# Kernel tuning notes

Measured on AMD Instinct MI355X. Metric: run time of the kernel, lower is better.

## Reference

```python
import jax, jax.numpy as jnp
import numpy as np

B, N, K = 32, 128, 16
F_ATOM, F_NEI, D = 256, 256, 256
H = 4
DK = D // H
NEG = -1e9
EPS = 1e-5
SLOPE = 0.2  # LeakyReLU slope (GAT convention)


def setup_inputs() -> dict:
    key = jax.random.key(0)
    ks = jax.random.split(key, 10)
    atom_feature = jax.random.normal(ks[0], (B, N, F_ATOM), jnp.float32)
    atom_neighbor_feature = jax.random.normal(ks[1], (B, N, K, F_NEI), jnp.float32)
    keep = (jax.random.uniform(ks[2], (B, N, K, 1)) < 0.8).astype(jnp.float32)
    atom_softmax_mask = (keep - 1.0) * (-NEG)  # 0 where valid, -1e9 where padded
    atom_attend_mask = keep
    s_a = 1.0 / np.sqrt(F_ATOM)
    s_n = 1.0 / np.sqrt(F_NEI)
    s_al = 1.0 / np.sqrt(DK)
    return {
        "atom_feature": atom_feature,
        "atom_neighbor_feature": atom_neighbor_feature,
        "atom_softmax_mask": atom_softmax_mask,
        "atom_attend_mask": atom_attend_mask,
        "W_a": jax.random.uniform(ks[3], (D, F_ATOM), jnp.float32, -s_a, s_a),
        "b_a": jnp.zeros((D,), jnp.float32),
        "W_n": jax.random.uniform(ks[4], (D, F_NEI), jnp.float32, -s_n, s_n),
        "b_n": jnp.zeros((D,), jnp.float32),
        "w_align": jax.random.uniform(ks[5], (DK,), jnp.float32, -s_al, s_al),
        "b_align": jnp.zeros((), jnp.float32),
        "ln_gamma": jnp.ones((D,), jnp.float32),
        "ln_beta": jnp.zeros((D,), jnp.float32),
    }


def reference(atom_feature, atom_neighbor_feature, atom_softmax_mask,
              atom_attend_mask, W_a, b_a, W_n, b_n, w_align, b_align,
              ln_gamma, ln_beta):
    # Linear projections (dropout is identity at inference)
    af = jnp.einsum('bnf,df->bnd', atom_feature, W_a) + b_a            # [B,N,D]
    nf = jnp.einsum('bnkf,df->bnkd', atom_neighbor_feature, W_n) + b_n  # [B,N,K,D]
    b, n, k, d = nf.shape
    afh = af.reshape(b, n, 1, H, DK)      # broadcast over neighbor axis
    nfh = nf.reshape(b, n, k, H, DK)
    # GATV2: act(Wa x_i + Wn x_j) . a
    feat = jax.nn.leaky_relu(afh + nfh, SLOPE)                          # [B,N,K,H,DK]
    score = jnp.einsum('bnkhd,d->bnkh', feat, w_align) + b_align        # [B,N,K,H]
    score = score + atom_softmax_mask                                   # [B,N,K,1] -> bcast over H
    attw = jax.nn.softmax(score, axis=2)                                # softmax over neighbors
    attw = attw * atom_attend_mask                                      # zero out padded neighbors
    ctx = jnp.einsum('bnkh,bnkhd->bnhd', attw, nfh).reshape(b, n, d)    # weighted sum
    # LayerNorm
    mu = jnp.mean(ctx, axis=-1, keepdims=True)
    var = jnp.mean(jnp.square(ctx - mu), axis=-1, keepdims=True)
    out = (ctx - mu) * jax.lax.rsqrt(var + EPS) * ln_gamma + ln_beta
    return out
```

## Files before the change

### kernel.cpp

```cpp
#include <hip/hip_runtime.h>
#include <hip/hip_bf16.h>


typedef float f32x4 __attribute__((ext_vector_type(4)));
typedef __bf16 bf16x8 __attribute__((ext_vector_type(8)));

__device__ __forceinline__ unsigned short f2bf(float x) {
    unsigned int u = __float_as_uint(x);
    u += 0x7FFFu + ((u >> 16) & 1u);
    return (unsigned short)(u >> 16);
}

__device__ __forceinline__ void gemm_tile(const float4* __restrict__ src4,
                                          const unsigned short* __restrict__ w,
                                          char* lds_a, f32x4 acc[2][4]) {
    const int tid = threadIdx.x;
#pragma unroll
    for (int j = 0; j < 8; ++j) {
        const int idx4 = tid + j * 256;
        const float4 v = src4[idx4];
        const int r = idx4 >> 6;
        const int byt = (idx4 & 63) * 8;
        ushort4 h;
        h.x = f2bf(v.x); h.y = f2bf(v.y); h.z = f2bf(v.z); h.w = f2bf(v.w);
        *(ushort4*)(lds_a + r * 512 + (byt ^ ((r & 7) << 4))) = h;
    }
    __syncthreads();
    const int lane = tid & 63;
    const int wv   = tid >> 6;
    const int l15  = lane & 15;
    const int lg   = lane >> 4;
#pragma unroll
    for (int kk = 0; kk < 8; ++kk) {
        const int f = kk * 32 + lg * 8;
        bf16x8 afrag[2];
#pragma unroll
        for (int mi = 0; mi < 2; ++mi) {
            const int r = mi * 16 + l15;
            afrag[mi] = *(const bf16x8*)(lds_a + r * 512 + ((f * 2) ^ ((r & 7) << 4)));
        }
#pragma unroll
        for (int ni = 0; ni < 4; ++ni) {
            const int d = wv * 64 + ni * 16 + l15;
            const bf16x8 bfrag = *(const bf16x8*)(w + d * 256 + f);
#pragma unroll
            for (int mi = 0; mi < 2; ++mi)
                acc[mi][ni] = __builtin_amdgcn_mfma_f32_16x16x32_bf16(
                    afrag[mi], bfrag, acc[mi][ni], 0, 0, 0);
        }
    }
}

__global__ __launch_bounds__(256) void conv_w(const float4* __restrict__ wa,
                                              const float4* __restrict__ wn,
                                              ushort4* __restrict__ owa,
                                              ushort4* __restrict__ own) {
    const int i = blockIdx.x * 256 + threadIdx.x;
    const float4 a = wa[i], n = wn[i];
    ushort4 ha, hn;
    ha.x = f2bf(a.x); ha.y = f2bf(a.y); ha.z = f2bf(a.z); ha.w = f2bf(a.w);
    hn.x = f2bf(n.x); hn.y = f2bf(n.y); hn.z = f2bf(n.z); hn.w = f2bf(n.w);
    owa[i] = ha; own[i] = hn;
}

__global__ __launch_bounds__(256) void proj_atoms(const float* __restrict__ atomf,
                                                  const unsigned short* __restrict__ wa,
                                                  const float* __restrict__ b_a,
                                                  float* __restrict__ af) {
    __shared__ char lds[32 * 512];
    f32x4 acc[2][4];
#pragma unroll
    for (int mi = 0; mi < 2; ++mi)
#pragma unroll
        for (int ni = 0; ni < 4; ++ni)
#pragma unroll
            for (int j = 0; j < 4; ++j) acc[mi][ni][j] = 0.f;
    gemm_tile((const float4*)(atomf + blockIdx.x * 32 * 256), wa, lds, acc);
    const int lane = threadIdx.x & 63, wv = threadIdx.x >> 6;
    const int l15 = lane & 15, lg = lane >> 4;
#pragma unroll
    for (int ni = 0; ni < 4; ++ni) {
        const int d = wv * 64 + ni * 16 + l15;
        const float b = b_a[d];
#pragma unroll
        for (int mi = 0; mi < 2; ++mi)
#pragma unroll
            for (int j = 0; j < 4; ++j)
                af[(blockIdx.x * 32 + mi * 16 + lg * 4 + j) * 256 + d] = acc[mi][ni][j] + b;
    }
}

struct Smem2 {
    union {
        char  a[32 * 512];
        float nf[32][260];
    } u;
    float af[2][256];
    float wal[64];
    float attw[2][4][16];
    float red[4][2][2];
};

__global__ __launch_bounds__(256) void gat_fused(
        const float* __restrict__ nei, const float* __restrict__ afbuf,
        const unsigned short* __restrict__ wn, const float* __restrict__ b_n,
        const float* __restrict__ smask, const float* __restrict__ amask,
        const float* __restrict__ w_align, const float* __restrict__ b_align,
        const float* __restrict__ gamma, const float* __restrict__ beta,
        float* __restrict__ out) {
    __shared__ Smem2 s;
    const int tid = threadIdx.x;
    const int p = blockIdx.x;

    s.af[0][tid] = afbuf[p * 512 + tid];
    s.af[1][tid] = afbuf[p * 512 + 256 + tid];
    if (tid < 64) s.wal[tid] = w_align[tid];

    f32x4 acc[2][4];
#pragma unroll
    for (int mi = 0; mi < 2; ++mi)
#pragma unroll
        for (int ni = 0; ni < 4; ++ni)
#pragma unroll
            for (int j = 0; j < 4; ++j) acc[mi][ni][j] = 0.f;

    gemm_tile((const float4*)(nei + (size_t)p * 32 * 256), wn, s.u.a, acc);
    __syncthreads();

    const int lane = tid & 63, wv = tid >> 6, l15 = lane & 15, lg = lane >> 4;
#pragma unroll
    for (int ni = 0; ni < 4; ++ni) {
        const int d = wv * 64 + ni * 16 + l15;
        const float bn = b_n[d];
#pragma unroll
        for (int mi = 0; mi < 2; ++mi)
#pragma unroll
            for (int j = 0; j < 4; ++j)
                s.u.nf[mi * 16 + lg * 4 + j][d] = acc[mi][ni][j] + bn;
    }
    __syncthreads();

    if (tid < 128) {
        const int a = tid >> 6, h = (tid >> 4) & 3, k = tid & 15;
        const float* afr = &s.af[a][h * 64];
        const float* nfr = &s.u.nf[a * 16 + k][h * 64];
        float sc = 0.f;
#pragma unroll
        for (int dk = 0; dk < 64; ++dk) {
            float x = afr[dk] + nfr[dk];
            x = (x >= 0.f) ? x : 0.2f * x;
            sc = fmaf(x, s.wal[dk], sc);
        }
        sc += b_align[0] + smask[p * 32 + a * 16 + k];
        float mx = sc;
#pragma unroll
        for (int o = 1; o < 16; o <<= 1) mx = fmaxf(mx, __shfl_xor(mx, o));
        const float e = __expf(sc - mx);
        float sm = e;
#pragma unroll
        for (int o = 1; o < 16; o <<= 1) sm += __shfl_xor(sm, o);
        s.attw[a][h][k] = (e / sm) * amask[p * 32 + a * 16 + k];
    }
    __syncthreads();

    const int d = tid;
    const float g = gamma[d], be = beta[d];
    const int h = d >> 6;
#pragma unroll
    for (int a = 0; a < 2; ++a) {
        float c = 0.f;
#pragma unroll
        for (int k = 0; k < 16; ++k)
            c = fmaf(s.attw[a][h][k], s.u.nf[a * 16 + k][d], c);
        float sm = c, sq = c * c;
#pragma unroll
        for (int o = 1; o < 64; o <<= 1) {
            sm += __shfl_xor(sm, o);
            sq += __shfl_xor(sq, o);
        }
        if (lane == 0) { s.red[wv][a][0] = sm; s.red[wv][a][1] = sq; }
        __syncthreads();
        float ts = 0.f, tq = 0.f;
#pragma unroll
        for (int q = 0; q < 4; ++q) { ts += s.red[q][a][0]; tq += s.red[q][a][1]; }
        const float mu = ts * (1.f / 256.f);
        float var = tq * (1.f / 256.f) - mu * mu;
        var = fmaxf(var, 0.f);
        out[(p * 2 + a) * 256 + d] = (c - mu) * rsqrtf(var + 1e-5f) * g + be;
        __syncthreads();
    }
}

extern "C" void kernel_launch(void* const* d_in, const int* in_sizes, int n_in,
                              void* d_out, int out_size, void* d_ws, size_t ws_size,
                              hipStream_t stream) {
    const float* atomf = (const float*)d_in[0];
    const float* nei   = (const float*)d_in[1];
    const float* smask = (const float*)d_in[2];
    const float* amask = (const float*)d_in[3];
    const float* Wa    = (const float*)d_in[4];
    const float* ba    = (const float*)d_in[5];
    const float* Wn    = (const float*)d_in[6];
    const float* bn    = (const float*)d_in[7];
    const float* wal   = (const float*)d_in[8];
    const float* bal   = (const float*)d_in[9];
    const float* gam   = (const float*)d_in[10];
    const float* bet   = (const float*)d_in[11];
    float* out = (float*)d_out;

    char* ws = (char*)d_ws;
    float*          af_buf = (float*)ws;
    unsigned short* wa_bf  = (unsigned short*)(ws + 4194304);
    unsigned short* wn_bf  = (unsigned short*)(ws + 4194304 + 131072);

    hipLaunchKernelGGL(conv_w, dim3(64), dim3(256), 0, stream,
                       (const float4*)Wa, (const float4*)Wn,
                       (ushort4*)wa_bf, (ushort4*)wn_bf);
    hipLaunchKernelGGL(proj_atoms, dim3(128), dim3(256), 0, stream,
                       atomf, wa_bf, ba, af_buf);
    hipLaunchKernelGGL(gat_fused, dim3(2048), dim3(256), 0, stream,
                       nei, af_buf, wn_bf, bn, smask, amask, wal, bal, gam, bet, out);
}
```

Before: 162.3 us.

## Fuse atom projection into GAT kernel with pre-swizzled bf16 weight fragments

Drops the separate proj_atoms kernel and its global af buffer. Each block now projects its two atom rows in an extra MFMA row-tile, reading bf16 weights stored in MFMA fragment order and prefetching the next k-step's fragments into registers. It also vectorises the score loop with float4 LDS reads, merges the two LayerNorm passes so fewer barriers are needed, and pads the nf rows. The costs are extra MFMA work on a mostly empty 16-row tile (only 2 rows are valid) and higher register pressure, with a launch-bounds occupancy hint of 3.

```diff
diff --git a/kernel.cpp b/kernel.cpp
--- a/kernel.cpp
+++ b/kernel.cpp
@@ -11,10 +11,50 @@
     return (unsigned short)(u >> 16);
 }
 
-__device__ __forceinline__ void gemm_tile(const float4* __restrict__ src4,
-                                          const unsigned short* __restrict__ w,
-                                          char* lds_a, f32x4 acc[2][4]) {
+__global__ __launch_bounds__(256) void conv_w(const float* __restrict__ wa,
+                                              const float* __restrict__ wn,
+                                              unsigned short* __restrict__ owa,
+                                              unsigned short* __restrict__ own) {
+    const int g = blockIdx.x * 256 + threadIdx.x;
+    const float* src = (g & 8192) ? wn : wa;
+    unsigned short* dst = (g & 8192) ? own : owa;
+    const int c = g & 8191;
+    const int lane = c & 63, ni = (c >> 6) & 3, kk = (c >> 8) & 7, wv = c >> 11;
+    const int d = wv * 64 + ni * 16 + (lane & 15);
+    const int f = kk * 32 + (lane >> 4) * 8;
+    const float* sp = src + d * 256 + f;
+    unsigned short h[8];
+#pragma unroll
+    for (int j = 0; j < 8; ++j) h[j] = f2bf(sp[j]);
+    *(uint4*)(dst + c * 8) = *(const uint4*)h;
+}
+
+struct Smem2 {
+    union {
+        char  a[48 * 512];
+        float nf[32][264];
+    } u;
+    float af[2][256];
+    float wal[64];
+    float attw[2][4][16];
+    float red[4][2][2];
+};
+
+__global__ __launch_bounds__(256, 3) void gat_fused(
+        const float* __restrict__ atomf, const float* __restrict__ nei,
+        const unsigned short* __restrict__ wn_p, const unsigned short* __restrict__ wa_p,
+        const float* __restrict__ b_n, const float* __restrict__ b_a,
+        const float* __restrict__ smask, const float* __restrict__ amask,
+        const float* __restrict__ w_align, const float* __restrict__ b_align,
+        const float* __restrict__ gamma, const float* __restrict__ beta,
+        float* __restrict__ out) {
+    __shared__ Smem2 s;
     const int tid = threadIdx.x;
+    const int p = blockIdx.x;
+
+    if (tid < 64) s.wal[tid] = w_align[tid];
+
+    const float4* src4 = (const float4*)(nei + (size_t)p * 32 * 256);
 #pragma unroll
     for (int j = 0; j < 8; ++j) {
         const int idx4 = tid + j * 256;
@@ -23,133 +63,96 @@
         const int byt = (idx4 & 63) * 8;
         ushort4 h;
         h.x = f2bf(v.x); h.y = f2bf(v.y); h.z = f2bf(v.z); h.w = f2bf(v.w);
-        *(ushort4*)(lds_a + r * 512 + (byt ^ ((r & 7) << 4))) = h;
-    }
-    __syncthreads();
-    const int lane = tid & 63;
-    const int wv   = tid >> 6;
-    const int l15  = lane & 15;
-    const int lg   = lane >> 4;
+        *(ushort4*)(s.u.a + r * 512 + (byt ^ ((r & 7) << 4))) = h;
+    }
+    if (tid < 128) {
+        const int at = tid >> 6, cc = tid & 63;
+        const float4 v = *(const float4*)(atomf + (size_t)(p * 2 + at) * 256 + cc * 4);
+        const int r = 32 + at;
+        ushort4 h;
+        h.x = f2bf(v.x); h.y = f2bf(v.y); h.z = f2bf(v.z); h.w = f2bf(v.w);
+        *(ushort4*)(s.u.a + r * 512 + ((cc * 8) ^ ((r & 7) << 4))) = h;
+    }
+    __syncthreads();
+
+    const int lane = tid & 63, wv = tid >> 6, l15 = lane & 15, lg = lane >> 4;
+
+    f32x4 acc[3][4];
+#pragma unroll
+    for (int mi = 0; mi < 3; ++mi)
+#pragma unroll
+        for (int ni = 0; ni < 4; ++ni)
+#pragma unroll
+            for (int j = 0; j < 4; ++j) acc[mi][ni][j] = 0.f;
+
+    const unsigned short* wn_wv = wn_p + wv * 16384 + lane * 8;
+    const unsigned short* wa_wv = wa_p + wv * 16384 + lane * 8;
+    bf16x8 cn[4], ca[4];
+#pragma unroll
+    for (int ni = 0; ni < 4; ++ni) {
+        cn[ni] = *(const bf16x8*)(wn_wv + ni * 512);
+        ca[ni] = *(const bf16x8*)(wa_wv + ni * 512);
+    }
 #pragma unroll
     for (int kk = 0; kk < 8; ++kk) {
-        const int f = kk * 32 + lg * 8;
-        bf16x8 afrag[2];
-#pragma unroll
-        for (int mi = 0; mi < 2; ++mi) {
+        bf16x8 nn[4], na[4];
+        if (kk < 7) {
+#pragma unroll
+            for (int ni = 0; ni < 4; ++ni) {
+                nn[ni] = *(const bf16x8*)(wn_wv + (kk + 1) * 2048 + ni * 512);
+                na[ni] = *(const bf16x8*)(wa_wv + (kk + 1) * 2048 + ni * 512);
+            }
+        }
+        const int fb = (kk * 32 + lg * 8) * 2;
+        bf16x8 afr[3];
+#pragma unroll
+        for (int mi = 0; mi < 3; ++mi) {
             const int r = mi * 16 + l15;
-            afrag[mi] = *(const bf16x8*)(lds_a + r * 512 + ((f * 2) ^ ((r & 7) << 4)));
+            afr[mi] = *(const bf16x8*)(s.u.a + r * 512 + (fb ^ ((r & 7) << 4)));
         }
 #pragma unroll
         for (int ni = 0; ni < 4; ++ni) {
-            const int d = wv * 64 + ni * 16 + l15;
-            const bf16x8 bfrag = *(const bf16x8*)(w + d * 256 + f);
-#pragma unroll
-            for (int mi = 0; mi < 2; ++mi)
-                acc[mi][ni] = __builtin_amdgcn_mfma_f32_16x16x32_bf16(
-                    afrag[mi], bfrag, acc[mi][ni], 0, 0, 0);
-        }
-    }
-}
-
-__global__ __launch_bounds__(256) void conv_w(const float4* __restrict__ wa,
-                                              const float4* __restrict__ wn,
-                                              ushort4* __restrict__ owa,
-                                              ushort4* __restrict__ own) {
-    const int i = blockIdx.x * 256 + threadIdx.x;
-    const float4 a = wa[i], n = wn[i];
-    ushort4 ha, hn;
-    ha.x = f2bf(a.x); ha.y = f2bf(a.y); ha.z = f2bf(a.z); ha.w = f2bf(a.w);
-    hn.x = f2bf(n.x); hn.y = f2bf(n.y); hn.z = f2bf(n.z); hn.w = f2bf(n.w);
-    owa[i] = ha; own[i] = hn;
-}
-
-__global__ __launch_bounds__(256) void proj_atoms(const float* __restrict__ atomf,
-                                                  const unsigned short* __restrict__ wa,
-                                                  const float* __restrict__ b_a,
-                                                  float* __restrict__ af) {
-    __shared__ char lds[32 * 512];
-    f32x4 acc[2][4];
-#pragma unroll
-    for (int mi = 0; mi < 2; ++mi)
-#pragma unroll
-        for (int ni = 0; ni < 4; ++ni)
-#pragma unroll
-            for (int j = 0; j < 4; ++j) acc[mi][ni][j] = 0.f;
-    gemm_tile((const float4*)(atomf + blockIdx.x * 32 * 256), wa, lds, acc);
-    const int lane = threadIdx.x & 63, wv = threadIdx.x >> 6;
-    const int l15 = lane & 15, lg = lane >> 4;
+            acc[0][ni] = __builtin_amdgcn_mfma_f32_16x16x32_bf16(afr[0], cn[ni], acc[0][ni], 0, 0, 0);
+            acc[1][ni] = __builtin_amdgcn_mfma_f32_16x16x32_bf16(afr[1], cn[ni], acc[1][ni], 0, 0, 0);
+            acc[2][ni] = __builtin_amdgcn_mfma_f32_16x16x32_bf16(afr[2], ca[ni], acc[2][ni], 0, 0, 0);
+        }
+        if (kk < 7) {
+#pragma unroll
+            for (int ni = 0; ni < 4; ++ni) { cn[ni] = nn[ni]; ca[ni] = na[ni]; }
+        }
+    }
+    __syncthreads();
+
 #pragma unroll
     for (int ni = 0; ni < 4; ++ni) {
         const int d = wv * 64 + ni * 16 + l15;
-        const float b = b_a[d];
-#pragma unroll
-        for (int mi = 0; mi < 2; ++mi)
-#pragma unroll
-            for (int j = 0; j < 4; ++j)
-                af[(blockIdx.x * 32 + mi * 16 + lg * 4 + j) * 256 + d] = acc[mi][ni][j] + b;
-    }
-}
-
-struct Smem2 {
-    union {
-        char  a[32 * 512];
-        float nf[32][260];
-    } u;
-    float af[2][256];
-    float wal[64];
-    float attw[2][4][16];
-    float red[4][2][2];
-};
-
-__global__ __launch_bounds__(256) void gat_fused(
-        const float* __restrict__ nei, const float* __restrict__ afbuf,
-        const unsigned short* __restrict__ wn, const float* __restrict__ b_n,
-        const float* __restrict__ smask, const float* __restrict__ amask,
-        const float* __restrict__ w_align, const float* __restrict__ b_align,
-        const float* __restrict__ gamma, const float* __restrict__ beta,
-        float* __restrict__ out) {
-    __shared__ Smem2 s;
-    const int tid = threadIdx.x;
-    const int p = blockIdx.x;
-
-    s.af[0][tid] = afbuf[p * 512 + tid];
-    s.af[1][tid] = afbuf[p * 512 + 256 + tid];
-    if (tid < 64) s.wal[tid] = w_align[tid];
-
-    f32x4 acc[2][4];
-#pragma unroll
-    for (int mi = 0; mi < 2; ++mi)
-#pragma unroll
-        for (int ni = 0; ni < 4; ++ni)
-#pragma unroll
-            for (int j = 0; j < 4; ++j) acc[mi][ni][j] = 0.f;
-
-    gemm_tile((const float4*)(nei + (size_t)p * 32 * 256), wn, s.u.a, acc);
-    __syncthreads();
-
-    const int lane = tid & 63, wv = tid >> 6, l15 = lane & 15, lg = lane >> 4;
-#pragma unroll
-    for (int ni = 0; ni < 4; ++ni) {
-        const int d = wv * 64 + ni * 16 + l15;
-        const float bn = b_n[d];
-#pragma unroll
-        for (int mi = 0; mi < 2; ++mi)
-#pragma unroll
-            for (int j = 0; j < 4; ++j)
-                s.u.nf[mi * 16 + lg * 4 + j][d] = acc[mi][ni][j] + bn;
+        const float bnv = b_n[d], bav = b_a[d];
+#pragma unroll
+        for (int j = 0; j < 4; ++j) {
+            s.u.nf[lg * 4 + j][d]      = acc[0][ni][j] + bnv;
+            s.u.nf[16 + lg * 4 + j][d] = acc[1][ni][j] + bnv;
+        }
+        if (lg == 0) {
+            s.af[0][d] = acc[2][ni][0] + bav;
+            s.af[1][d] = acc[2][ni][1] + bav;
+        }
     }
     __syncthreads();
 
     if (tid < 128) {
         const int a = tid >> 6, h = (tid >> 4) & 3, k = tid & 15;
-        const float* afr = &s.af[a][h * 64];
-        const float* nfr = &s.u.nf[a * 16 + k][h * 64];
+        const float4* af4 = (const float4*)(&s.af[a][h * 64]);
+        const float4* nf4 = (const float4*)(&s.u.nf[a * 16 + k][h * 64]);
+        const float4* wl4 = (const float4*)(s.wal);
         float sc = 0.f;
 #pragma unroll
-        for (int dk = 0; dk < 64; ++dk) {
-            float x = afr[dk] + nfr[dk];
-            x = (x >= 0.f) ? x : 0.2f * x;
-            sc = fmaf(x, s.wal[dk], sc);
+        for (int i = 0; i < 16; ++i) {
+            const float4 x = af4[i], y = nf4[i], w = wl4[i];
+            float z0 = x.x + y.x, z1 = x.y + y.y, z2 = x.z + y.z, z3 = x.w + y.w;
+            z0 = fmaxf(z0, 0.2f * z0); z1 = fmaxf(z1, 0.2f * z1);
+            z2 = fmaxf(z2, 0.2f * z2); z3 = fmaxf(z3, 0.2f * z3);
+            sc = fmaf(z0, w.x, sc); sc = fmaf(z1, w.y, sc);
+            sc = fmaf(z2, w.z, sc); sc = fmaf(z3, w.w, sc);
         }
         sc += b_align[0] + smask[p * 32 + a * 16 + k];
         float mx = sc;
@@ -163,32 +166,35 @@
     }
     __syncthreads();
 
-    const int d = tid;
+    const int d = tid, hh = d >> 6;
+    float c0 = 0.f, c1 = 0.f;
+#pragma unroll
+    for (int k = 0; k < 16; ++k) c0 = fmaf(s.attw[0][hh][k], s.u.nf[k][d], c0);
+#pragma unroll
+    for (int k = 0; k < 16; ++k) c1 = fmaf(s.attw[1][hh][k], s.u.nf[16 + k][d], c1);
+    float sm0 = c0, sq0 = c0 * c0, sm1 = c1, sq1 = c1 * c1;
+#pragma unroll
+    for (int o = 1; o < 64; o <<= 1) {
+        sm0 += __shfl_xor(sm0, o); sq0 += __shfl_xor(sq0, o);
+        sm1 += __shfl_xor(sm1, o); sq1 += __shfl_xor(sq1, o);
+    }
+    if (lane == 0) {
+        s.red[wv][0][0] = sm0; s.red[wv][0][1] = sq0;
+        s.red[wv][1][0] = sm1; s.red[wv][1][1] = sq1;
+    }
+    __syncthreads();
+    float ts0 = 0.f, tq0 = 0.f, ts1 = 0.f, tq1 = 0.f;
+#pragma unroll
+    for (int q = 0; q < 4; ++q) {
+        ts0 += s.red[q][0][0]; tq0 += s.red[q][0][1];
+        ts1 += s.red[q][1][0]; tq1 += s.red[q][1][1];
+    }
     const float g = gamma[d], be = beta[d];
-    const int h = d >> 6;
-#pragma unroll
-    for (int a = 0; a < 2; ++a) {
-        float c = 0.f;
-#pragma unroll
-        for (int k = 0; k < 16; ++k)
-            c = fmaf(s.attw[a][h][k], s.u.nf[a * 16 + k][d], c);
-        float sm = c, sq = c * c;
-#pragma unroll
-        for (int o = 1; o < 64; o <<= 1) {
-            sm += __shfl_xor(sm, o);
-            sq += __shfl_xor(sq, o);
-        }
-        if (lane == 0) { s.red[wv][a][0] = sm; s.red[wv][a][1] = sq; }
-        __syncthreads();
-        float ts = 0.f, tq = 0.f;
-#pragma unroll
-        for (int q = 0; q < 4; ++q) { ts += s.red[q][a][0]; tq += s.red[q][a][1]; }
-        const float mu = ts * (1.f / 256.f);
-        float var = tq * (1.f / 256.f) - mu * mu;
-        var = fmaxf(var, 0.f);
-        out[(p * 2 + a) * 256 + d] = (c - mu) * rsqrtf(var + 1e-5f) * g + be;
-        __syncthreads();
-    }
+    const float mu0 = ts0 * (1.f / 256.f), mu1 = ts1 * (1.f / 256.f);
+    const float v0 = fmaxf(tq0 * (1.f / 256.f) - mu0 * mu0, 0.f);
+    const float v1 = fmaxf(tq1 * (1.f / 256.f) - mu1 * mu1, 0.f);
+    out[(size_t)(p * 2) * 256 + d]     = (c0 - mu0) * rsqrtf(v0 + 1e-5f) * g + be;
+    out[(size_t)(p * 2 + 1) * 256 + d] = (c1 - mu1) * rsqrtf(v1 + 1e-5f) * g + be;
 }
 
 extern "C" void kernel_launch(void* const* d_in, const int* in_sizes, int n_in,
@@ -209,15 +215,12 @@
     float* out = (float*)d_out;
 
     char* ws = (char*)d_ws;
-    float*          af_buf = (float*)ws;
-    unsigned short* wa_bf  = (unsigned short*)(ws + 4194304);
-    unsigned short* wn_bf  = (unsigned short*)(ws + 4194304 + 131072);
+    unsigned short* wa_bf = (unsigned short*)ws;
+    unsigned short* wn_bf = (unsigned short*)(ws + 131072);
 
     hipLaunchKernelGGL(conv_w, dim3(64), dim3(256), 0, stream,
-                       (const float4*)Wa, (const float4*)Wn,
-                       (ushort4*)wa_bf, (ushort4*)wn_bf);
-    hipLaunchKernelGGL(proj_atoms, dim3(128), dim3(256), 0, stream,
-                       atomf, wa_bf, ba, af_buf);
+                       Wa, Wn, wa_bf, wn_bf);
     hipLaunchKernelGGL(gat_fused, dim3(2048), dim3(256), 0, stream,
-                       nei, af_buf, wn_bf, bn, smask, amask, wal, bal, gam, bet, out);
-}
+                       atomf, nei, wn_bf, wa_bf, bn, ba, smask, amask,
+                       wal, bal, gam, bet, out);
+}
```

Result: faster. 142.8 us (-12.0%).
